# Kernel optimization log

Hardware: AMD Instinct MI355X
Metric: run time of the kernel (lower is better)

The kernel has to match this reference:

```python
import jax, jax.numpy as jnp
import numpy as np

N = 100000   # total nodes
E = 800000   # edges (before self loops)
B = 64       # graphs in batch
NF = 9       # node features
HID = 128    # gnn hidden
HEADS = 4
HC = HID // HEADS  # 32 per-head channels
L = 4        # gnn layers
SEQ = 768    # seq embed dim
HD = 256     # fusion hidden dim
AH = 4       # cross-attn heads
LN_EPS = 1e-5


def setup_inputs() -> dict:
    key = jax.random.key(0)
    ks = jax.random.split(key, 40)
    rn = lambda k, s, sc=0.05: jax.random.normal(k, s, jnp.float32) * sc
    inp = {}
    inp['seq_embedding'] = jax.random.normal(ks[0], (B, SEQ), jnp.float32)
    inp['x'] = jax.random.uniform(ks[1], (N, NF), jnp.float32)
    inp['edge_index'] = jax.random.randint(ks[2], (2, E), 0, N, jnp.int32)
    inp['batch'] = jnp.sort(jax.random.randint(ks[3], (N,), 0, B, jnp.int32))
    # node embed MLP
    inp['ne_W'] = rn(ks[4], (HID, NF)); inp['ne_b'] = rn(ks[5], (HID,))
    # GAT layers (stacked over L)
    inp['gat_W'] = rn(ks[6], (L, HID, HID))          # lin weight (out,in) per layer
    inp['gat_asrc'] = rn(ks[7], (L, HEADS, HC))
    inp['gat_adst'] = rn(ks[8], (L, HEADS, HC))
    inp['gat_b'] = rn(ks[9], (L, HID))
    inp['ln_g'] = jnp.ones((L, HID), jnp.float32)
    inp['ln_b'] = jnp.zeros((L, HID), jnp.float32)
    # gnn output projection
    inp['op1_W'] = rn(ks[10], (HID, HID)); inp['op1_b'] = rn(ks[11], (HID,))
    inp['op2_W'] = rn(ks[12], (HID, HID)); inp['op2_b'] = rn(ks[13], (HID,))
    # fusion projections
    inp['sp_W'] = rn(ks[14], (HD, SEQ)); inp['sp_b'] = rn(ks[15], (HD,))
    inp['stp_W'] = rn(ks[16], (HD, HID)); inp['stp_b'] = rn(ks[17], (HD,))
    # two MultiheadAttention blocks (torch layout: in_proj (3D,D), out_proj (D,D))
    inp['a1_Wi'] = rn(ks[18], (3 * HD, HD)); inp['a1_bi'] = rn(ks[19], (3 * HD,))
    inp['a1_Wo'] = rn(ks[20], (HD, HD)); inp['a1_bo'] = rn(ks[21], (HD,))
    inp['a2_Wi'] = rn(ks[22], (3 * HD, HD)); inp['a2_bi'] = rn(ks[23], (3 * HD,))
    inp['a2_Wo'] = rn(ks[24], (HD, HD)); inp['a2_bo'] = rn(ks[25], (HD,))
    # predictor MLP: 4*HD -> HD -> HD/2 -> 1
    inp['p1_W'] = rn(ks[26], (HD, 4 * HD)); inp['p1_b'] = rn(ks[27], (HD,))
    inp['p2_W'] = rn(ks[28], (HD // 2, HD)); inp['p2_b'] = rn(ks[29], (HD // 2,))
    inp['p3_W'] = rn(ks[30], (1, HD // 2)); inp['p3_b'] = rn(ks[31], (1,))
    return inp


def _gat_layer(x, src, dst, W, a_src, a_dst, bias):
    # PyG GATConv: shared lin, per-head additive attention, scatter softmax over dst.
    n = x.shape[0]
    xl = (x @ W.T).reshape(n, HEADS, HC)                      # [N,H,C]
    e_src = jnp.einsum('nhc,hc->nh', xl, a_src)
    e_dst = jnp.einsum('nhc,hc->nh', xl, a_dst)
    e = jax.nn.leaky_relu(e_src[src] + e_dst[dst], 0.2)       # [Et,H]
    m = jax.ops.segment_max(e, dst, num_segments=n)           # stable softmax
    p = jnp.exp(e - m[dst])
    s = jax.ops.segment_sum(p, dst, num_segments=n)
    alpha = p / (s[dst] + 1e-16)
    msg = xl[src] * alpha[:, :, None]                         # [Et,H,C]
    out = jax.ops.segment_sum(msg, dst, num_segments=n)
    return out.reshape(n, HID) + bias


def _layernorm(x, g, b):
    mu = jnp.mean(x, -1, keepdims=True)
    var = jnp.mean(jnp.square(x - mu), -1, keepdims=True)
    return (x - mu) * jax.lax.rsqrt(var + LN_EPS) * g + b


def _mha(q, k, v, Wi, bi, Wo, bo):
    # torch MultiheadAttention, batch_first, q/k/v: [B,1,HD]
    Wq, Wk, Wv = Wi[:HD], Wi[HD:2 * HD], Wi[2 * HD:]
    bq, bk, bv = bi[:HD], bi[HD:2 * HD], bi[2 * HD:]
    def heads(t, Wt, bt):
        return (t @ Wt.T + bt).reshape(t.shape[0], t.shape[1], AH, HD // AH)
    qh, kh, vh = heads(q, Wq, bq), heads(k, Wk, bk), heads(v, Wv, bv)
    scores = jnp.einsum('bqhd,bkhd->bhqk', qh, kh) / jnp.sqrt(jnp.float32(HD // AH))
    attn = jax.nn.softmax(scores, axis=-1)
    o = jnp.einsum('bhqk,bkhd->bqhd', attn, vh).reshape(q.shape[0], q.shape[1], HD)
    return o @ Wo.T + bo


def reference(seq_embedding, x, edge_index, batch,
              ne_W, ne_b, gat_W, gat_asrc, gat_adst, gat_b, ln_g, ln_b,
              op1_W, op1_b, op2_W, op2_b, sp_W, sp_b, stp_W, stp_b,
              a1_Wi, a1_bi, a1_Wo, a1_bo, a2_Wi, a2_bi, a2_Wo, a2_bo,
              p1_W, p1_b, p2_W, p2_b, p3_W, p3_b):
    n = x.shape[0]
    loops = jnp.arange(n, dtype=edge_index.dtype)
    src = jnp.concatenate([edge_index[0], loops])   # add_self_loops (PyG default)
    dst = jnp.concatenate([edge_index[1], loops])
    # node embed (dropout = identity in eval)
    h = jax.nn.relu(x @ ne_W.T + ne_b)
    for l in range(L):
        hn = _gat_layer(h, src, dst, gat_W[l], gat_asrc[l], gat_adst[l], gat_b[l])
        hn = jax.nn.relu(_layernorm(hn, ln_g[l], ln_b[l]))
        h = h + hn
    # global mean pool
    sums = jax.ops.segment_sum(h, batch, num_segments=B)
    cnts = jax.ops.segment_sum(jnp.ones((n,), h.dtype), batch, num_segments=B)
    pooled = sums / jnp.maximum(cnts, 1.0)[:, None]
    struct_emb = jax.nn.relu(pooled @ op1_W.T + op1_b) @ op2_W.T + op2_b
    # fusion
    seq_h = (seq_embedding @ sp_W.T + sp_b)[:, None, :]       # [B,1,HD]
    struct_h = (struct_emb @ stp_W.T + stp_b)[:, None, :]
    seq_att = _mha(seq_h, struct_h, struct_h, a1_Wi, a1_bi, a1_Wo, a1_bo)[:, 0]
    struct_att = _mha(struct_h, seq_h, seq_h, a2_Wi, a2_bi, a2_Wo, a2_bo)[:, 0]
    comb = jnp.concatenate([seq_att, struct_att, seq_h[:, 0], struct_h[:, 0]], -1)
    z = jax.nn.relu(comb @ p1_W.T + p1_b)
    z = jax.nn.relu(z @ p2_W.T + p2_b)
    return (z @ p3_W.T + p3_b)[:, 0]
```

## Files before the change

kernel.cpp:

```cpp
#include <hip/hip_runtime.h>
#include <hip/hip_bf16.h>

#define N_NODES 100000
#define NFEAT 9
#define HID 128
#define B_GRAPHS 64
#define SEQ_LEN 768
#define HD 256
#define L_LAYERS 4
#define LN_EPS 1e-5f

typedef __attribute__((ext_vector_type(8))) short short8;
typedef __attribute__((ext_vector_type(4))) float f32x4;

__device__ __forceinline__ float lrelu(float v) { return v > 0.f ? v : 0.2f * v; }

__device__ __forceinline__ float wave_sum64(float x) {
#pragma unroll
  for (int o = 32; o >= 1; o >>= 1) x += __shfl_xor(x, o, 64);
  return x;
}

__device__ __forceinline__ unsigned short bf16r(float v) {
  unsigned int u = __float_as_uint(v);
  return (unsigned short)((u + 0x7fffu + ((u >> 16) & 1u)) >> 16);
}
__device__ __forceinline__ unsigned int bf16pair(float lo, float hi) {
  unsigned int ul = __float_as_uint(lo);
  unsigned int uh = __float_as_uint(hi);
  ul = (ul + 0x7fffu + ((ul >> 16) & 1u)) >> 16;
  uh = (uh + 0x7fffu + ((uh >> 16) & 1u)) & 0xffff0000u;
  return ul | uh;
}
__device__ __forceinline__ float bflo(unsigned int u) { return __uint_as_float(u << 16); }
__device__ __forceinline__ float bfhi(unsigned int u) { return __uint_as_float(u & 0xffff0000u); }

__global__ __launch_bounds__(256) void ne_kernel(const float* __restrict__ x,
                                                 const float* __restrict__ W,
                                                 const float* __restrict__ b,
                                                 unsigned short* __restrict__ hb) {
  int idx = blockIdx.x * 256 + threadIdx.x;
  int n = idx >> 7, c = idx & 127;
  const float* xr = x + n * NFEAT;
  const float* wr = W + c * NFEAT;
  float acc = b[c];
#pragma unroll
  for (int k = 0; k < NFEAT; ++k) acc += xr[k] * wr[k];
  acc = fmaxf(acc, 0.f);
  hb[idx] = bf16r(acc);
}

__global__ __launch_bounds__(256) void wcvt_kernel(const float* __restrict__ W,
                                                   unsigned short* __restrict__ wb) {
  int idx = blockIdx.x * 256 + threadIdx.x;
  if (idx < L_LAYERS * HID * HID) wb[idx] = bf16r(W[idx]);
}

__global__ __launch_bounds__(256) void wprep_kernel(const float* __restrict__ W,
                                                    const float* __restrict__ asrc,
                                                    const float* __restrict__ adst,
                                                    unsigned short* __restrict__ was8) {
  int t = blockIdx.x * 256 + threadIdx.x;
  if (t >= L_LAYERS * 16 * 128) return;
  int l = t >> 11;
  int rem = t & 2047;
  int j = rem >> 7;
  int k = rem & 127;
  float sum = 0.f;
  if (j < 8) {
    int head = j & 3;
    const float* a = (j < 4) ? (asrc + l * HID + head * 32) : (adst + l * HID + head * 32);
    const float* Wl = W + (size_t)l * HID * HID + (size_t)(head * 32) * HID + k;
#pragma unroll 8
    for (int c = 0; c < 32; ++c) sum += Wl[(size_t)c * HID] * a[c];
  }
  was8[t] = bf16r(sum);
}

__global__ __launch_bounds__(256) void hist_kernel(const int* __restrict__ dst,
                                                   int* __restrict__ cnt, int E) {
  int i = blockIdx.x * 256 + threadIdx.x;
  if (i < E) atomicAdd(&cnt[dst[i]], 1);
}

__global__ __launch_bounds__(1024) void scan1_kernel(const int* __restrict__ cnt,
                                                     int* __restrict__ off,
                                                     int* __restrict__ bsum, int n) {
  __shared__ int ws[16];
  __shared__ int wx[16];
  int tid = threadIdx.x, lane = tid & 63, w = tid >> 6;
  int i = blockIdx.x * 1024 + tid;
  int v = (i < n) ? cnt[i] : 0;
  int x = v;
#pragma unroll
  for (int o = 1; o < 64; o <<= 1) {
    int t = __shfl_up(x, o, 64);
    if (lane >= o) x += t;
  }
  if (lane == 63) ws[w] = x;
  __syncthreads();
  if (tid == 0) {
    int r = 0;
#pragma unroll
    for (int j = 0; j < 16; ++j) { int t = ws[j]; wx[j] = r; r += t; }
    bsum[blockIdx.x] = r;
  }
  __syncthreads();
  if (i < n) off[i] = wx[w] + x - v;
}

__global__ void scan2_kernel(int* __restrict__ bsum, int nb) {
  int lane = threadIdx.x;
  int i0 = lane * 2, i1 = i0 + 1;
  int a = (i0 < nb) ? bsum[i0] : 0;
  int b = (i1 < nb) ? bsum[i1] : 0;
  int s = a + b, x = s;
#pragma unroll
  for (int o = 1; o < 64; o <<= 1) {
    int t = __shfl_up(x, o, 64);
    if (lane >= o) x += t;
  }
  int excl = x - s;
  if (i0 < nb) bsum[i0] = excl;
  if (i1 < nb) bsum[i1] = excl + a;
}

__global__ __launch_bounds__(256) void scan3_kernel(const int* __restrict__ bsum,
                                                    int* __restrict__ off, int n, int total) {
  int i = blockIdx.x * 256 + threadIdx.x;
  if (i < n) off[i] += bsum[i >> 10];
  else if (i == n) off[i] = total;
}

__global__ __launch_bounds__(256) void scatter_kernel(const int* __restrict__ src,
                                                      const int* __restrict__ dst,
                                                      const int* __restrict__ off,
                                                      int* __restrict__ cur,
                                                      int* __restrict__ eadj, int E) {
  int i = blockIdx.x * 256 + threadIdx.x;
  if (i < E) {
    int d = dst[i];
    int pos = atomicAdd(&cur[d], 1);
    eadj[off[d] + pos] = src[i] << 8;
  }
}

__device__ __forceinline__ int csr_row_of(const int* __restrict__ off, int j, int lo, int hi) {
  while (lo + 1 < hi) {
    int mid = (lo + hi) >> 1;
    if (off[mid] <= j) lo = mid; else hi = mid;
  }
  return lo;
}

__global__ __launch_bounds__(256) void edgew_kernel(const int* __restrict__ eadj,
                                                    const int* __restrict__ off,
                                                    const float* __restrict__ esrc,
                                                    const float* __restrict__ edst,
                                                    uint2* __restrict__ qw, int E) {
  __shared__ int sLo, sHi;
  int tid = threadIdx.x;
  int j = blockIdx.x * 256 + tid;
  int jlast = min(blockIdx.x * 256 + 255, E - 1);
  if (tid == 0) sLo = csr_row_of(off, blockIdx.x * 256, 0, N_NODES);
  if (tid == 255) sHi = csr_row_of(off, jlast, 0, N_NODES) + 1;
  __syncthreads();
  if (j >= E) return;
  int d = csr_row_of(off, j, sLo, sHi);
  int sx = eadj[j];
  const float4 es = *(const float4*)(esrc + (sx >> 6));
  const float4 ed = *(const float4*)(edst + (size_t)d * 4);
  float q0 = __expf(lrelu(es.x + ed.x));
  float q1 = __expf(lrelu(es.y + ed.y));
  float q2 = __expf(lrelu(es.z + ed.z));
  float q3 = __expf(lrelu(es.w + ed.w));
  qw[j] = make_uint2(bf16pair(q0, q1), bf16pair(q2, q3));
}

__global__ __launch_bounds__(256) void gat_xl_kernel(const unsigned short* __restrict__ hb,
                                                     const unsigned short* __restrict__ wb,
                                                     const unsigned short* __restrict__ wasb,
                                                     unsigned int* __restrict__ xlp,
                                                     float* __restrict__ esrc,
                                                     float* __restrict__ edst) {
  __shared__ unsigned short Wl[128][136];
  const int tid = threadIdx.x;
  const int lane = tid & 63;
  const int wv = tid >> 6;
  const int base = blockIdx.x * 128;
  const int l15 = lane & 15;
  const int lg = lane >> 4;

#pragma unroll
  for (int t = 0; t < 8; ++t) {
    int f8 = tid + t * 256;
    int row = f8 >> 4, c8 = (f8 & 15) * 8;
    uint4 v = *(const uint4*)(wb + row * HID + c8);
    *(uint4*)&Wl[row][c8] = v;
  }
  __syncthreads();

  f32x4 acc[2][8];
  f32x4 acc_e[2];
#pragma unroll
  for (int rb = 0; rb < 2; ++rb) {
#pragma unroll
    for (int nb = 0; nb < 8; ++nb) acc[rb][nb] = (f32x4){0.f, 0.f, 0.f, 0.f};
    acc_e[rb] = (f32x4){0.f, 0.f, 0.f, 0.f};
  }

  int n0 = base + wv * 32 + l15;
  int n1 = n0 + 16;
  if (n0 >= N_NODES) n0 = N_NODES - 1;
  if (n1 >= N_NODES) n1 = N_NODES - 1;
  const size_t rowA0 = (size_t)n0 * HID;
  const size_t rowA1 = (size_t)n1 * HID;

#pragma unroll
  for (int kc = 0; kc < 4; ++kc) {
    const int kb = kc * 32 + lg * 8;
    short8 a0 = *(const short8*)(hb + rowA0 + kb);
    short8 a1 = *(const short8*)(hb + rowA1 + kb);
    short8 efrag = *(const short8*)(wasb + l15 * HID + kb);
    acc_e[0] = __builtin_amdgcn_mfma_f32_16x16x32_bf16(a0, efrag, acc_e[0], 0, 0, 0);
    acc_e[1] = __builtin_amdgcn_mfma_f32_16x16x32_bf16(a1, efrag, acc_e[1], 0, 0, 0);
#pragma unroll
    for (int nb = 0; nb < 8; ++nb) {
      short8 bfrag = *(const short8*)&Wl[nb * 16 + l15][kb];
      acc[0][nb] = __builtin_amdgcn_mfma_f32_16x16x32_bf16(a0, bfrag, acc[0][nb], 0, 0, 0);
      acc[1][nb] = __builtin_amdgcn_mfma_f32_16x16x32_bf16(a1, bfrag, acc[1][nb], 0, 0, 0);
    }
  }

#pragma unroll
  for (int rb = 0; rb < 2; ++rb) {
#pragma unroll
    for (int r = 0; r < 4; ++r) {
      int node = base + wv * 32 + rb * 16 + lg * 4 + r;
      if (node < N_NODES) {
#pragma unroll
        for (int nb = 0; nb < 4; ++nb) {
          unsigned int pk = bf16pair(acc[rb][nb][r], acc[rb][nb + 4][r]);
          xlp[(size_t)node * 64 + nb * 16 + l15] = pk;
        }
        float ev = acc_e[rb][r];
        if (l15 < 4) esrc[node * 4 + l15] = ev;
        else if (l15 < 8) edst[node * 4 + (l15 - 4)] = ev;
      }
    }
  }
}

__global__ __launch_bounds__(256) void gat_agg_kernel(const unsigned int* __restrict__ xlp,
                                                      const float* __restrict__ esrc,
                                                      const float* __restrict__ edst,
                                                      const uint2* __restrict__ qw,
                                                      const int* __restrict__ off,
                                                      const int* __restrict__ eadj,
                                                      const float* __restrict__ gbias,
                                                      const float* __restrict__ lng,
                                                      const float* __restrict__ lnb,
                                                      unsigned short* __restrict__ hb) {
  const int tid = threadIdx.x;
  const int lane = tid & 63;
  const int i = blockIdx.x * 4 + (tid >> 6);
  const int hd0 = lane >> 5;
  const unsigned int shA = hd0 ? 0u : 16u;

  const float4 ed = *(const float4*)(edst + (size_t)i * 4);
  const float4 e0 = *(const float4*)(esrc + (size_t)i * 4);
  float w0 = __expf(lrelu(e0.x + ed.x));
  float w1 = __expf(lrelu(e0.y + ed.y));
  float w2 = __expf(lrelu(e0.z + ed.z));
  float w3 = __expf(lrelu(e0.w + ed.w));
  float sA = (hd0 == 0 ? w0 : w1);
  float sB = (hd0 == 0 ? w2 : w3);
  const char* xpb = (const char*)xlp + (lane << 2);
  const unsigned int vi = *(const unsigned int*)(xpb + ((unsigned)i << 8));
  float accA = bflo(vi) * sA;
  float accB = bfhi(vi) * sB;

  const int beg = off[i], end = off[i + 1];
  int j = beg;
  int4 ea;
  uint2 Qa, Qb, Qc, Qd;
  if (j + 4 <= end) {
    ea = *(const int4*)(eadj + j);
    Qa = qw[j + 0]; Qb = qw[j + 1]; Qc = qw[j + 2]; Qd = qw[j + 3];
  }
  for (; j + 4 <= end;) {
    const unsigned int va = *(const unsigned int*)(xpb + (unsigned)ea.x);
    const unsigned int vb = *(const unsigned int*)(xpb + (unsigned)ea.y);
    const unsigned int vc = *(const unsigned int*)(xpb + (unsigned)ea.z);
    const unsigned int vd = *(const unsigned int*)(xpb + (unsigned)ea.w);
    int4 eaN;
    uint2 QaN, QbN, QcN, QdN;
    const int jn = j + 4;
    const bool more = jn + 4 <= end;
    if (more) {
      eaN = *(const int4*)(eadj + jn);
      QaN = qw[jn + 0]; QbN = qw[jn + 1]; QcN = qw[jn + 2]; QdN = qw[jn + 3];
    }
    float qAa = __uint_as_float((Qa.x << shA) & 0xffff0000u);
    float qBa = __uint_as_float((Qa.y << shA) & 0xffff0000u);
    float qAb = __uint_as_float((Qb.x << shA) & 0xffff0000u);
    float qBb = __uint_as_float((Qb.y << shA) & 0xffff0000u);
    float qAc = __uint_as_float((Qc.x << shA) & 0xffff0000u);
    float qBc = __uint_as_float((Qc.y << shA) & 0xffff0000u);
    float qAd = __uint_as_float((Qd.x << shA) & 0xffff0000u);
    float qBd = __uint_as_float((Qd.y << shA) & 0xffff0000u);
    sA += qAa + qAb + qAc + qAd;
    sB += qBa + qBb + qBc + qBd;
    accA = fmaf(bflo(va), qAa, accA);
    accA = fmaf(bflo(vb), qAb, accA);
    accA = fmaf(bflo(vc), qAc, accA);
    accA = fmaf(bflo(vd), qAd, accA);
    accB = fmaf(bfhi(va), qBa, accB);
    accB = fmaf(bfhi(vb), qBb, accB);
    accB = fmaf(bfhi(vc), qBc, accB);
    accB = fmaf(bfhi(vd), qBd, accB);
    if (more) { ea = eaN; Qa = QaN; Qb = QbN; Qc = QcN; Qd = QdN; }
    j = jn;
  }
  for (; j < end; ++j) {
    const int sx = eadj[j];
    const uint2 Q = qw[j];
    const unsigned int v = *(const unsigned int*)(xpb + (unsigned)sx);
    float qA = __uint_as_float((Q.x << shA) & 0xffff0000u);
    float qB = __uint_as_float((Q.y << shA) & 0xffff0000u);
    sA += qA;
    sB += qB;
    accA = fmaf(bflo(v), qA, accA);
    accB = fmaf(bfhi(v), qB, accB);
  }
  float o0 = accA / (sA + 1e-16f) + gbias[lane];
  float o1 = accB / (sB + 1e-16f) + gbias[lane + 64];
  float s1 = o0 + o1;
  float s2 = o0 * o0 + o1 * o1;
#pragma unroll
  for (int o = 32; o >= 1; o >>= 1) {
    s1 += __shfl_xor(s1, o, 64);
    s2 += __shfl_xor(s2, o, 64);
  }
  float mu = s1 * (1.f / 128.f);
  float var = fmaxf(s2 * (1.f / 128.f) - mu * mu, 0.f);
  float r = rsqrtf(var + LN_EPS);
  float d0 = o0 - mu, d1 = o1 - mu;
  float hn0 = fmaxf(d0 * r * lng[lane] + lnb[lane], 0.f);
  float hn1 = fmaxf(d1 * r * lng[lane + 64] + lnb[lane + 64], 0.f);
  unsigned short h0 = hb[(size_t)i * HID + lane];
  unsigned short h1 = hb[(size_t)i * HID + 64 + lane];
  float nh0 = __uint_as_float((unsigned int)h0 << 16) + hn0;
  float nh1 = __uint_as_float((unsigned int)h1 << 16) + hn1;
  hb[(size_t)i * HID + lane] = bf16r(nh0);
  hb[(size_t)i * HID + 64 + lane] = bf16r(nh1);
}

__device__ __forceinline__ int lower_bound_dev(const int* a, int n, int v) {
  int lo = 0, hi = n;
  while (lo < hi) {
    int mid = (lo + hi) >> 1;
    if (a[mid] < v) lo = mid + 1; else hi = mid;
  }
  return lo;
}

__global__ __launch_bounds__(256) void pool_kernel(const unsigned short* __restrict__ hb,
                                                   const int* __restrict__ batch,
                                                   float* __restrict__ pooled) {
  __shared__ float red[256];
  int b = blockIdx.x, tid = threadIdx.x;
  int start = lower_bound_dev(batch, N_NODES, b);
  int end = lower_bound_dev(batch, N_NODES, b + 1);
  int cl = tid & 31, g = tid >> 5;
  int c = cl + blockIdx.y * 32;
  float acc = 0.f;
  for (int n = start + g; n < end; n += 8)
    acc += __uint_as_float((unsigned int)hb[(size_t)n * HID + c] << 16);
  red[tid] = acc;
  __syncthreads();
  if (g == 0) {
    float tot = 0.f;
#pragma unroll
    for (int k = 0; k < 8; ++k) tot += red[cl + 32 * k];
    float cntf = fmaxf((float)(end - start), 1.f);
    pooled[b * HID + c] = tot / cntf;
  }
}

__global__ __launch_bounds__(256) void gemv2_kernel(
    const float* __restrict__ A1, int lda1, const float* __restrict__ W1,
    const float* __restrict__ b1, float* __restrict__ O1, int ldo1,
    int sh1, int K1, int relu1,
    const float* __restrict__ A2, int lda2, const float* __restrict__ W2,
    const float* __restrict__ b2, float* __restrict__ O2, int ldo2,
    int sh2, int K2, int relu2, int nw1, int nwTot) {
  int gw = (blockIdx.x * 256 + threadIdx.x) >> 6;
  int lane = threadIdx.x & 63;
  if (gw >= nwTot) return;
  const float *A, *W, *b;
  float* O;
  int lda, ldo, K, relu, m, c;
  if (gw < nw1) {
    A = A1; W = W1; b = b1; O = O1; lda = lda1; ldo = ldo1; K = K1; relu = relu1;
    m = gw >> sh1; c = gw & ((1 << sh1) - 1);
  } else {
    int g2 = gw - nw1;
    A = A2; W = W2; b = b2; O = O2; lda = lda2; ldo = ldo2; K = K2; relu = relu2;
    m = g2 >> sh2; c = g2 & ((1 << sh2) - 1);
  }
  const float* a = A + (size_t)m * lda;
  const float* w = W + (size_t)c * K;
  float acc = 0.f;
  for (int k = lane * 2; k < K; k += 128) {
    float2 av = *(const float2*)(a + k);
    float2 wv = *(const float2*)(w + k);
    acc += av.x * wv.x + av.y * wv.y;
  }
  acc = wave_sum64(acc);
  if (lane == 0) {
    acc += b[c];
    if (relu) acc = fmaxf(acc, 0.f);
    O[(size_t)m * ldo + c] = acc;
  }
}

__global__ __launch_bounds__(256) void z1_kernel(const float* __restrict__ att1,
                                                 const float* __restrict__ att2,
                                                 const float* __restrict__ seqh,
                                                 const float* __restrict__ strh,
                                                 const float* __restrict__ p1_W,
                                                 const float* __restrict__ p1_b,
                                                 float* __restrict__ z1) {
  int gw = (blockIdx.x * 256 + threadIdx.x) >> 6;
  int lane = threadIdx.x & 63;
  int m = gw >> 8, c = gw & 255;
  const float* segs[4] = {att1 + m * HD, att2 + m * HD, seqh + m * HD, strh + m * HD};
  const float* w = p1_W + (size_t)c * (4 * HD);
  float acc = 0.f;
#pragma unroll
  for (int s = 0; s < 4; ++s) {
    const float* a = segs[s];
#pragma unroll
    for (int k = lane * 2; k < HD; k += 128) {
      float2 av = *(const float2*)(a + k);
      float2 wv = *(const float2*)(w + s * HD + k);
      acc += av.x * wv.x + av.y * wv.y;
    }
  }
  acc = wave_sum64(acc);
  if (lane == 0) z1[m * HD + c] = fmaxf(acc + p1_b[c], 0.f);
}

extern "C" void kernel_launch(void* const* d_in, const int* in_sizes, int n_in,
                              void* d_out, int out_size, void* d_ws, size_t ws_size,
                              hipStream_t stream) {
  const float* seq_emb = (const float*)d_in[0];
  const float* x       = (const float*)d_in[1];
  const int* eidx      = (const int*)d_in[2];
  const int* batch     = (const int*)d_in[3];
  const float* ne_W = (const float*)d_in[4];
  const float* ne_b = (const float*)d_in[5];
  const float* gat_W = (const float*)d_in[6];
  const float* gat_asrc = (const float*)d_in[7];
  const float* gat_adst = (const float*)d_in[8];
  const float* gat_b = (const float*)d_in[9];
  const float* ln_g = (const float*)d_in[10];
  const float* ln_b = (const float*)d_in[11];
  const float* op1_W = (const float*)d_in[12];
  const float* op1_b = (const float*)d_in[13];
  const float* op2_W = (const float*)d_in[14];
  const float* op2_b = (const float*)d_in[15];
  const float* sp_W = (const float*)d_in[16];
  const float* sp_b = (const float*)d_in[17];
  const float* stp_W = (const float*)d_in[18];
  const float* stp_b = (const float*)d_in[19];
  const float* a1_Wi = (const float*)d_in[20];
  const float* a1_bi = (const float*)d_in[21];
  const float* a1_Wo = (const float*)d_in[22];
  const float* a1_bo = (const float*)d_in[23];
  const float* a2_Wi = (const float*)d_in[24];
  const float* a2_bi = (const float*)d_in[25];
  const float* a2_Wo = (const float*)d_in[26];
  const float* a2_bo = (const float*)d_in[27];
  const float* p1_W = (const float*)d_in[28];
  const float* p1_b = (const float*)d_in[29];
  const float* p2_W = (const float*)d_in[30];
  const float* p2_b = (const float*)d_in[31];
  const float* p3_W = (const float*)d_in[32];
  const float* p3_b = (const float*)d_in[33];

  const int E = in_sizes[2] / 2;
  const int* e_src = eidx;
  const int* e_dst = eidx + E;

  char* p = (char*)d_ws;
  auto alloc = [&](size_t bytes) -> void* {
    void* r = p;
    p += (bytes + 255) & ~(size_t)255;
    return r;
  };
  unsigned short* hbuf = (unsigned short*)alloc(sizeof(unsigned short) * (size_t)N_NODES * HID);
  unsigned short* wb   = (unsigned short*)alloc(sizeof(unsigned short) * L_LAYERS * HID * HID);
  unsigned short* was8 = (unsigned short*)alloc(sizeof(unsigned short) * L_LAYERS * 16 * HID);
  unsigned int* xlp = (unsigned int*)alloc(sizeof(unsigned int) * (size_t)N_NODES * 64);
  float* esrc = (float*)alloc(sizeof(float) * (size_t)N_NODES * 4);
  float* edst = (float*)alloc(sizeof(float) * (size_t)N_NODES * 4);
  int* cnt    = (int*)alloc(sizeof(int) * N_NODES);
  int* cur    = (int*)alloc(sizeof(int) * N_NODES);
  int* off    = (int*)alloc(sizeof(int) * (N_NODES + 1));
  int* eadj   = (int*)alloc(sizeof(int) * (size_t)E);
  uint2* qw   = (uint2*)alloc(sizeof(uint2) * (size_t)E);
  int* bsum   = (int*)alloc(sizeof(int) * 128);
  float* pooled = (float*)alloc(sizeof(float) * B_GRAPHS * HID);
  float* t1B   = (float*)alloc(sizeof(float) * B_GRAPHS * HID);
  float* sembB = (float*)alloc(sizeof(float) * B_GRAPHS * HID);
  float* seqhB = (float*)alloc(sizeof(float) * B_GRAPHS * HD);
  float* strhB = (float*)alloc(sizeof(float) * B_GRAPHS * HD);
  float* v1B   = (float*)alloc(sizeof(float) * B_GRAPHS * HD);
  float* v2B   = (float*)alloc(sizeof(float) * B_GRAPHS * HD);
  float* att1B = (float*)alloc(sizeof(float) * B_GRAPHS * HD);
  float* att2B = (float*)alloc(sizeof(float) * B_GRAPHS * HD);
  float* z1B   = (float*)alloc(sizeof(float) * B_GRAPHS * HD);
  float* z2B   = (float*)alloc(sizeof(float) * B_GRAPHS * (HD / 2));

  hipMemsetAsync(cnt, 0, sizeof(int) * N_NODES, stream);
  hipMemsetAsync(cur, 0, sizeof(int) * N_NODES, stream);

  const int SCAN_BLKS = (N_NODES + 1023) / 1024;
  ne_kernel<<<N_NODES * HID / 256, 256, 0, stream>>>(x, ne_W, ne_b, hbuf);
  wcvt_kernel<<<(L_LAYERS * HID * HID + 255) / 256, 256, 0, stream>>>(gat_W, wb);
  wprep_kernel<<<(L_LAYERS * 16 * 128 + 255) / 256, 256, 0, stream>>>(gat_W, gat_asrc, gat_adst, was8);
  hist_kernel<<<(E + 255) / 256, 256, 0, stream>>>(e_dst, cnt, E);
  scan1_kernel<<<SCAN_BLKS, 1024, 0, stream>>>(cnt, off, bsum, N_NODES);
  scan2_kernel<<<1, 64, 0, stream>>>(bsum, SCAN_BLKS);
  scan3_kernel<<<(N_NODES + 256) / 256, 256, 0, stream>>>(bsum, off, N_NODES, E);
  scatter_kernel<<<(E + 255) / 256, 256, 0, stream>>>(e_src, e_dst, off, cur, eadj, E);

  const unsigned EDGE_BLKS = (E + 255) / 256;
  for (int l = 0; l < L_LAYERS; ++l) {
    gat_xl_kernel<<<(N_NODES + 127) / 128, 256, 0, stream>>>(
        hbuf, wb + (size_t)l * HID * HID, was8 + (size_t)l * 16 * HID,
        xlp, esrc, edst);
    edgew_kernel<<<EDGE_BLKS, 256, 0, stream>>>(eadj, off, esrc, edst, qw, E);
    gat_agg_kernel<<<N_NODES / 4, 256, 0, stream>>>(
        xlp, esrc, edst, qw, off, eadj, gat_b + l * HID, ln_g + l * HID, ln_b + l * HID,
        hbuf);
  }
  pool_kernel<<<dim3(B_GRAPHS, 4), 256, 0, stream>>>(hbuf, batch, pooled);

  const float* a1_Wv = a1_Wi + 2 * HD * HD;
  const float* a1_bv = a1_bi + 2 * HD;
  const float* a2_Wv = a2_Wi + 2 * HD * HD;
  const float* a2_bv = a2_bi + 2 * HD;
  auto nblk = [](int waves) { return (unsigned)((waves + 3) / 4); };

  {
    int nw1 = B_GRAPHS * HD, nwT = nw1 + B_GRAPHS * HID;
    gemv2_kernel<<<nblk(nwT), 256, 0, stream>>>(
        seq_emb, SEQ_LEN, sp_W, sp_b, seqhB, HD, 8, SEQ_LEN, 0,
        pooled, HID, op1_W, op1_b, t1B, HID, 7, HID, 1, nw1, nwT);
  }
  {
    int nw1 = B_GRAPHS * HD, nwT = nw1 + B_GRAPHS * HID;
    gemv2_kernel<<<nblk(nwT), 256, 0, stream>>>(
        seqhB, HD, a2_Wv, a2_bv, v2B, HD, 8, HD, 0,
        t1B, HID, op2_W, op2_b, sembB, HID, 7, HID, 0, nw1, nwT);
  }
  {
    int nw1 = B_GRAPHS * HD, nwT = nw1 + B_GRAPHS * HD;
    gemv2_kernel<<<nblk(nwT), 256, 0, stream>>>(
        v2B, HD, a2_Wo, a2_bo, att2B, HD, 8, HD, 0,
        sembB, HID, stp_W, stp_b, strhB, HD, 8, HID, 0, nw1, nwT);
  }
  {
    int nwT = B_GRAPHS * HD;
    gemv2_kernel<<<nblk(nwT), 256, 0, stream>>>(
        strhB, HD, a1_Wv, a1_bv, v1B, HD, 8, HD, 0,
        nullptr, 0, nullptr, nullptr, nullptr, 0, 0, 0, 0, nwT, nwT);
  }
  {
    int nwT = B_GRAPHS * HD;
    gemv2_kernel<<<nblk(nwT), 256, 0, stream>>>(
        v1B, HD, a1_Wo, a1_bo, att1B, HD, 8, HD, 0,
        nullptr, 0, nullptr, nullptr, nullptr, 0, 0, 0, 0, nwT, nwT);
  }
  z1_kernel<<<nblk(B_GRAPHS * HD), 256, 0, stream>>>(att1B, att2B, seqhB, strhB, p1_W, p1_b, z1B);
  {
    int nwT = B_GRAPHS * (HD / 2);
    gemv2_kernel<<<nblk(nwT), 256, 0, stream>>>(
        z1B, HD, p2_W, p2_b, z2B, HD / 2, 7, HD, 1,
        nullptr, 0, nullptr, nullptr, nullptr, 0, 0, 0, 0, nwT, nwT);
  }
  {
    int nwT = B_GRAPHS;
    gemv2_kernel<<<nblk(nwT), 256, 0, stream>>>(
        z2B, HD / 2, p3_W, p3_b, (float*)d_out, 1, 0, HD / 2, 0,
        nullptr, 0, nullptr, nullptr, nullptr, 0, 0, 0, 0, nwT, nwT);
  }
}
```

Measured before the change: 612.4 us.

## Process two nodes per wavefront in GAT aggregation with 8-byte gathers

Each 64-lane wave now handles two destination nodes, with 32 lanes per node and each lane gathering a uint2 holding 4 bf16 channels instead of one 32-bit word. The scalar remainder loop is replaced by a single masked 4-wide tail, and eadj/qw are padded so the tail can over-read safely. The aim is fewer waves, wider memory transactions and more edge parallelism per wave. In exchange the explicit software prefetch of the next edge batch is dropped, and each lane holds more accumulators.

```diff
diff --git a/kernel.cpp b/kernel.cpp
--- a/kernel.cpp
+++ b/kernel.cpp
@@ -263,97 +263,140 @@
                                                       unsigned short* __restrict__ hb) {
   const int tid = threadIdx.x;
   const int lane = tid & 63;
-  const int i = blockIdx.x * 4 + (tid >> 6);
-  const int hd0 = lane >> 5;
-  const unsigned int shA = hd0 ? 0u : 16u;
-
-  const float4 ed = *(const float4*)(edst + (size_t)i * 4);
-  const float4 e0 = *(const float4*)(esrc + (size_t)i * 4);
-  float w0 = __expf(lrelu(e0.x + ed.x));
-  float w1 = __expf(lrelu(e0.y + ed.y));
-  float w2 = __expf(lrelu(e0.z + ed.z));
-  float w3 = __expf(lrelu(e0.w + ed.w));
-  float sA = (hd0 == 0 ? w0 : w1);
-  float sB = (hd0 == 0 ? w2 : w3);
-  const char* xpb = (const char*)xlp + (lane << 2);
-  const unsigned int vi = *(const unsigned int*)(xpb + ((unsigned)i << 8));
-  float accA = bflo(vi) * sA;
-  float accB = bfhi(vi) * sB;
-
-  const int beg = off[i], end = off[i + 1];
+  const int hl = lane & 31;
+  const int half = lane >> 5;
+  const int node = blockIdx.x * 8 + (tid >> 6) * 2 + half;
+  const int h0 = hl >> 4;
+  const unsigned int shQ = h0 ? 0u : 16u;
+
+  const float4 es = *(const float4*)(esrc + (size_t)node * 4);
+  const float4 ed = *(const float4*)(edst + (size_t)node * 4);
+  float wA = __expf(lrelu(h0 ? (es.y + ed.y) : (es.x + ed.x)));
+  float wB = __expf(lrelu(h0 ? (es.w + ed.w) : (es.z + ed.z)));
+  float sA = wA, sB = wB;
+  const char* xpb = (const char*)xlp + (hl << 3);
+  const uint2 vi = *(const uint2*)(xpb + ((unsigned)node << 8));
+  float acc0 = bflo(vi.x) * wA;
+  float acc1 = bflo(vi.y) * wA;
+  float acc2 = bfhi(vi.x) * wB;
+  float acc3 = bfhi(vi.y) * wB;
+
+  const int beg = off[node], end = off[node + 1];
   int j = beg;
-  int4 ea;
-  uint2 Qa, Qb, Qc, Qd;
-  if (j + 4 <= end) {
-    ea = *(const int4*)(eadj + j);
-    Qa = qw[j + 0]; Qb = qw[j + 1]; Qc = qw[j + 2]; Qd = qw[j + 3];
-  }
-  for (; j + 4 <= end;) {
-    const unsigned int va = *(const unsigned int*)(xpb + (unsigned)ea.x);
-    const unsigned int vb = *(const unsigned int*)(xpb + (unsigned)ea.y);
-    const unsigned int vc = *(const unsigned int*)(xpb + (unsigned)ea.z);
-    const unsigned int vd = *(const unsigned int*)(xpb + (unsigned)ea.w);
-    int4 eaN;
-    uint2 QaN, QbN, QcN, QdN;
-    const int jn = j + 4;
-    const bool more = jn + 4 <= end;
-    if (more) {
-      eaN = *(const int4*)(eadj + jn);
-      QaN = qw[jn + 0]; QbN = qw[jn + 1]; QcN = qw[jn + 2]; QdN = qw[jn + 3];
-    }
-    float qAa = __uint_as_float((Qa.x << shA) & 0xffff0000u);
-    float qBa = __uint_as_float((Qa.y << shA) & 0xffff0000u);
-    float qAb = __uint_as_float((Qb.x << shA) & 0xffff0000u);
-    float qBb = __uint_as_float((Qb.y << shA) & 0xffff0000u);
-    float qAc = __uint_as_float((Qc.x << shA) & 0xffff0000u);
-    float qBc = __uint_as_float((Qc.y << shA) & 0xffff0000u);
-    float qAd = __uint_as_float((Qd.x << shA) & 0xffff0000u);
-    float qBd = __uint_as_float((Qd.y << shA) & 0xffff0000u);
-    sA += qAa + qAb + qAc + qAd;
-    sB += qBa + qBb + qBc + qBd;
-    accA = fmaf(bflo(va), qAa, accA);
-    accA = fmaf(bflo(vb), qAb, accA);
-    accA = fmaf(bflo(vc), qAc, accA);
-    accA = fmaf(bflo(vd), qAd, accA);
-    accB = fmaf(bfhi(va), qBa, accB);
-    accB = fmaf(bfhi(vb), qBb, accB);
-    accB = fmaf(bfhi(vc), qBc, accB);
-    accB = fmaf(bfhi(vd), qBd, accB);
-    if (more) { ea = eaN; Qa = QaN; Qb = QbN; Qc = QcN; Qd = QdN; }
-    j = jn;
-  }
-  for (; j < end; ++j) {
-    const int sx = eadj[j];
-    const uint2 Q = qw[j];
-    const unsigned int v = *(const unsigned int*)(xpb + (unsigned)sx);
-    float qA = __uint_as_float((Q.x << shA) & 0xffff0000u);
-    float qB = __uint_as_float((Q.y << shA) & 0xffff0000u);
-    sA += qA;
-    sB += qB;
-    accA = fmaf(bflo(v), qA, accA);
-    accB = fmaf(bfhi(v), qB, accB);
-  }
-  float o0 = accA / (sA + 1e-16f) + gbias[lane];
-  float o1 = accB / (sB + 1e-16f) + gbias[lane + 64];
-  float s1 = o0 + o1;
-  float s2 = o0 * o0 + o1 * o1;
-#pragma unroll
-  for (int o = 32; o >= 1; o >>= 1) {
+  for (; j + 4 <= end; j += 4) {
+    const int4 ea = *(const int4*)(eadj + j);
+    const uint2 Q0 = qw[j + 0];
+    const uint2 Q1 = qw[j + 1];
+    const uint2 Q2 = qw[j + 2];
+    const uint2 Q3 = qw[j + 3];
+    const uint2 v0 = *(const uint2*)(xpb + (unsigned)ea.x);
+    const uint2 v1 = *(const uint2*)(xpb + (unsigned)ea.y);
+    const uint2 v2 = *(const uint2*)(xpb + (unsigned)ea.z);
+    const uint2 v3 = *(const uint2*)(xpb + (unsigned)ea.w);
+    float qA0 = __uint_as_float((Q0.x << shQ) & 0xffff0000u);
+    float qB0 = __uint_as_float((Q0.y << shQ) & 0xffff0000u);
+    float qA1 = __uint_as_float((Q1.x << shQ) & 0xffff0000u);
+    float qB1 = __uint_as_float((Q1.y << shQ) & 0xffff0000u);
+    float qA2 = __uint_as_float((Q2.x << shQ) & 0xffff0000u);
+    float qB2 = __uint_as_float((Q2.y << shQ) & 0xffff0000u);
+    float qA3 = __uint_as_float((Q3.x << shQ) & 0xffff0000u);
+    float qB3 = __uint_as_float((Q3.y << shQ) & 0xffff0000u);
+    sA += qA0 + qA1 + qA2 + qA3;
+    sB += qB0 + qB1 + qB2 + qB3;
+    acc0 = fmaf(bflo(v0.x), qA0, acc0);
+    acc1 = fmaf(bflo(v0.y), qA0, acc1);
+    acc2 = fmaf(bfhi(v0.x), qB0, acc2);
+    acc3 = fmaf(bfhi(v0.y), qB0, acc3);
+    acc0 = fmaf(bflo(v1.x), qA1, acc0);
+    acc1 = fmaf(bflo(v1.y), qA1, acc1);
+    acc2 = fmaf(bfhi(v1.x), qB1, acc2);
+    acc3 = fmaf(bfhi(v1.y), qB1, acc3);
+    acc0 = fmaf(bflo(v2.x), qA2, acc0);
+    acc1 = fmaf(bflo(v2.y), qA2, acc1);
+    acc2 = fmaf(bfhi(v2.x), qB2, acc2);
+    acc3 = fmaf(bfhi(v2.y), qB2, acc3);
+    acc0 = fmaf(bflo(v3.x), qA3, acc0);
+    acc1 = fmaf(bflo(v3.y), qA3, acc1);
+    acc2 = fmaf(bfhi(v3.x), qB3, acc2);
+    acc3 = fmaf(bfhi(v3.y), qB3, acc3);
+  }
+  if (j < end) {
+    const int4 ea = *(const int4*)(eadj + j);
+    const uint2 Q0 = qw[j + 0];
+    const uint2 Q1 = qw[j + 1];
+    const uint2 Q2 = qw[j + 2];
+    const uint2 Q3 = qw[j + 3];
+    const uint2 v0 = *(const uint2*)(xpb + (unsigned)ea.x);
+    const uint2 v1 = *(const uint2*)(xpb + (unsigned)ea.y);
+    const uint2 v2 = *(const uint2*)(xpb + (unsigned)ea.z);
+    const uint2 v3 = *(const uint2*)(xpb + (unsigned)ea.w);
+    float qA0 = __uint_as_float((Q0.x << shQ) & 0xffff0000u);
+    float qB0 = __uint_as_float((Q0.y << shQ) & 0xffff0000u);
+    float qA1 = __uint_as_float((Q1.x << shQ) & 0xffff0000u);
+    float qB1 = __uint_as_float((Q1.y << shQ) & 0xffff0000u);
+    float qA2 = __uint_as_float((Q2.x << shQ) & 0xffff0000u);
+    float qB2 = __uint_as_float((Q2.y << shQ) & 0xffff0000u);
+    float qA3 = __uint_as_float((Q3.x << shQ) & 0xffff0000u);
+    float qB3 = __uint_as_float((Q3.y << shQ) & 0xffff0000u);
+    const int r = end - j;
+    if (r < 2) { qA1 = 0.f; qB1 = 0.f; }
+    if (r < 3) { qA2 = 0.f; qB2 = 0.f; }
+    qA3 = 0.f; qB3 = 0.f;
+    sA += qA0 + qA1 + qA2 + qA3;
+    sB += qB0 + qB1 + qB2 + qB3;
+    acc0 = fmaf(bflo(v0.x), qA0, acc0);
+    acc1 = fmaf(bflo(v0.y), qA0, acc1);
+    acc2 = fmaf(bfhi(v0.x), qB0, acc2);
+    acc3 = fmaf(bfhi(v0.y), qB0, acc3);
+    acc0 = fmaf(bflo(v1.x), qA1, acc0);
+    acc1 = fmaf(bflo(v1.y), qA1, acc1);
+    acc2 = fmaf(bfhi(v1.x), qB1, acc2);
+    acc3 = fmaf(bfhi(v1.y), qB1, acc3);
+    acc0 = fmaf(bflo(v2.x), qA2, acc0);
+    acc1 = fmaf(bflo(v2.y), qA2, acc1);
+    acc2 = fmaf(bfhi(v2.x), qB2, acc2);
+    acc3 = fmaf(bfhi(v2.y), qB2, acc3);
+    acc0 = fmaf(bflo(v3.x), qA3, acc0);
+    acc1 = fmaf(bflo(v3.y), qA3, acc1);
+    acc2 = fmaf(bfhi(v3.x), qB3, acc2);
+    acc3 = fmaf(bfhi(v3.y), qB3, acc3);
+  }
+
+  const float invA = 1.f / (sA + 1e-16f);
+  const float invB = 1.f / (sB + 1e-16f);
+  const float2 gb0 = *(const float2*)(gbias + 2 * hl);
+  const float2 gb1 = *(const float2*)(gbias + 64 + 2 * hl);
+  float o0 = acc0 * invA + gb0.x;
+  float o1 = acc1 * invA + gb0.y;
+  float o2 = acc2 * invB + gb1.x;
+  float o3 = acc3 * invB + gb1.y;
+  float s1 = o0 + o1 + o2 + o3;
+  float s2 = o0 * o0 + o1 * o1 + o2 * o2 + o3 * o3;
+#pragma unroll
+  for (int o = 16; o >= 1; o >>= 1) {
     s1 += __shfl_xor(s1, o, 64);
     s2 += __shfl_xor(s2, o, 64);
   }
   float mu = s1 * (1.f / 128.f);
   float var = fmaxf(s2 * (1.f / 128.f) - mu * mu, 0.f);
-  float r = rsqrtf(var + LN_EPS);
-  float d0 = o0 - mu, d1 = o1 - mu;
-  float hn0 = fmaxf(d0 * r * lng[lane] + lnb[lane], 0.f);
-  float hn1 = fmaxf(d1 * r * lng[lane + 64] + lnb[lane + 64], 0.f);
-  unsigned short h0 = hb[(size_t)i * HID + lane];
-  unsigned short h1 = hb[(size_t)i * HID + 64 + lane];
-  float nh0 = __uint_as_float((unsigned int)h0 << 16) + hn0;
-  float nh1 = __uint_as_float((unsigned int)h1 << 16) + hn1;
-  hb[(size_t)i * HID + lane] = bf16r(nh0);
-  hb[(size_t)i * HID + 64 + lane] = bf16r(nh1);
+  float rn = rsqrtf(var + LN_EPS);
+  const float2 lg0 = *(const float2*)(lng + 2 * hl);
+  const float2 lg1 = *(const float2*)(lng + 64 + 2 * hl);
+  const float2 lb0 = *(const float2*)(lnb + 2 * hl);
+  const float2 lb1 = *(const float2*)(lnb + 64 + 2 * hl);
+  float hn0 = fmaxf((o0 - mu) * rn * lg0.x + lb0.x, 0.f);
+  float hn1 = fmaxf((o1 - mu) * rn * lg0.y + lb0.y, 0.f);
+  float hn2 = fmaxf((o2 - mu) * rn * lg1.x + lb1.x, 0.f);
+  float hn3 = fmaxf((o3 - mu) * rn * lg1.y + lb1.y, 0.f);
+  unsigned int* hrow = (unsigned int*)(hb + (size_t)node * HID);
+  unsigned int h01 = hrow[hl];
+  unsigned int h23 = hrow[32 + hl];
+  float nh0 = bflo(h01) + hn0;
+  float nh1 = bfhi(h01) + hn1;
+  float nh2 = bflo(h23) + hn2;
+  float nh3 = bfhi(h23) + hn3;
+  hrow[hl] = bf16pair(nh0, nh1);
+  hrow[32 + hl] = bf16pair(nh2, nh3);
 }
 
 __device__ __forceinline__ int lower_bound_dev(const int* a, int n, int v) {
@@ -509,8 +552,8 @@
   int* cnt    = (int*)alloc(sizeof(int) * N_NODES);
   int* cur    = (int*)alloc(sizeof(int) * N_NODES);
   int* off    = (int*)alloc(sizeof(int) * (N_NODES + 1));
-  int* eadj   = (int*)alloc(sizeof(int) * (size_t)E);
-  uint2* qw   = (uint2*)alloc(sizeof(uint2) * (size_t)E);
+  int* eadj   = (int*)alloc(sizeof(int) * ((size_t)E + 8));
+  uint2* qw   = (uint2*)alloc(sizeof(uint2) * ((size_t)E + 8));
   int* bsum   = (int*)alloc(sizeof(int) * 128);
   float* pooled = (float*)alloc(sizeof(float) * B_GRAPHS * HID);
   float* t1B   = (float*)alloc(sizeof(float) * B_GRAPHS * HID);
@@ -526,6 +569,7 @@
 
   hipMemsetAsync(cnt, 0, sizeof(int) * N_NODES, stream);
   hipMemsetAsync(cur, 0, sizeof(int) * N_NODES, stream);
+  hipMemsetAsync(eadj + E, 0, sizeof(int) * 8, stream);
 
   const int SCAN_BLKS = (N_NODES + 1023) / 1024;
   ne_kernel<<<N_NODES * HID / 256, 256, 0, stream>>>(x, ne_W, ne_b, hbuf);
@@ -543,7 +587,7 @@
         hbuf, wb + (size_t)l * HID * HID, was8 + (size_t)l * 16 * HID,
         xlp, esrc, edst);
     edgew_kernel<<<EDGE_BLKS, 256, 0, stream>>>(eadj, off, esrc, edst, qw, E);
-    gat_agg_kernel<<<N_NODES / 4, 256, 0, stream>>>(
+    gat_agg_kernel<<<N_NODES / 8, 256, 0, stream>>>(
         xlp, esrc, edst, qw, off, eadj, gat_b + l * HID, ln_g + l * HID, ln_b + l * HID,
         hbuf);
   }
```

After: 584.6 us. 4.5% less time.
